# Kernel tuning notes

Hardware: AMD Instinct MI355X
Metric: run time of the kernel (lower is better)

Reference implementation:

```python
import jax, jax.numpy as jnp
import numpy as np

B, S, E, H = 2, 2048, 512, 8
D = E // H  # head_dim = 64


def setup_inputs() -> dict:
    key = jax.random.key(0)
    ks = jax.random.split(key, 10)
    sc = 1.0 / np.sqrt(E)
    x = jax.random.normal(ks[0], (B, S, E), dtype=jnp.float32)
    # parent index per node: tree_structure[b][parent[b,i]] contains i
    parent = jax.random.randint(ks[1], (B, S), 0, S, dtype=jnp.int32)
    Wp = jax.random.normal(ks[2], (E, E), dtype=jnp.float32) * sc
    bp = jnp.zeros((E,), dtype=jnp.float32)
    Wc = jax.random.normal(ks[3], (E, E), dtype=jnp.float32) * sc
    bc = jnp.zeros((E,), dtype=jnp.float32)
    Ws = jax.random.normal(ks[4], (E, E), dtype=jnp.float32) * sc
    bs = jnp.zeros((E,), dtype=jnp.float32)
    Wo = jax.random.normal(ks[5], (E, E), dtype=jnp.float32) * sc
    bo = jnp.zeros((E,), dtype=jnp.float32)
    return {"x": x, "parent": parent, "Wp": Wp, "bp": bp, "Wc": Wc,
            "bc": bc, "Ws": Ws, "bs": bs, "Wo": Wo, "bo": bo}


def _tree_mask(parent):
    # Vectorized equivalent of the per-batch scatter loop:
    # mask[b, p, c] = mask[b, c, p] = 1 for each (parent, child) edge.
    b_idx = jnp.arange(B)[:, None]
    rows = jnp.arange(S)[None, :]
    m = jnp.zeros((B, S, S), dtype=bool)
    m = m.at[b_idx, rows, parent].set(True)
    m = m.at[b_idx, parent, rows].set(True)
    return m  # (B, S, S), broadcast over heads


def reference(x, parent, Wp, bp, Wc, bc, Ws, bs, Wo, bo):
    # Tri-projection
    p = (x @ Wp + bp).reshape(B, S, H, D)
    c = (x @ Wc + bc).reshape(B, S, H, D)
    s = (x @ Ws + bs).reshape(B, S, H, D)
    scores = jnp.einsum('bnhd,bmhd->bnhm', p, c) / jnp.sqrt(jnp.float32(D))
    mask = _tree_mask(parent)  # (B, S, S)
    scores = jnp.where(mask[:, :, None, :], scores, -jnp.inf)
    attn = jax.nn.softmax(scores, axis=-1)  # dropout is identity (train=False)
    out = jnp.einsum('bnhm,bmhd->bnhd', attn, s).reshape(B, S, E)
    return out @ Wo + bo
```

## Files before the change

kernel.cpp:

```cpp
#include <hip/hip_runtime.h>
#include <hip/hip_bf16.h>

#define B_  2
#define S_  2048
#define E_  512
#define H_  8
#define D_  64
#define BS_ (B_ * S_)
#define N1_ 1536
#define K_  512

typedef __bf16 bf16x8 __attribute__((ext_vector_type(8)));
typedef float  f32x4  __attribute__((ext_vector_type(4)));

__device__ __forceinline__ ushort f2bf(float f) {
    unsigned u = __float_as_uint(f);
    unsigned r = (u + 0x7FFFu + ((u >> 16) & 1u)) >> 16;
    return (ushort)r;
}
__device__ __forceinline__ float bf2f(ushort b) {
    return __uint_as_float(((unsigned)b) << 16);
}

__device__ __forceinline__ float wave_sum(float v) {
    #pragma unroll
    for (int off = 32; off; off >>= 1) v += __shfl_xor(v, off);
    return v;
}

__device__ __forceinline__ void gld_lds16(const ushort* g, ushort* l) {
    __builtin_amdgcn_global_load_lds(
        (const __attribute__((address_space(1))) unsigned int*)g,
        (__attribute__((address_space(3))) unsigned int*)l, 16, 0, 0);
}


__global__ void convert_x_kernel(const float* __restrict__ x,
                                 ushort* __restrict__ xb, int n4) {
    int i = blockIdx.x * blockDim.x + threadIdx.x;
    if (i >= n4) return;
    float4 v = ((const float4*)x)[i];
    ushort4 o;
    o.x = f2bf(v.x); o.y = f2bf(v.y); o.z = f2bf(v.z); o.w = f2bf(v.w);
    ((ushort4*)xb)[i] = o;
}

__global__ __launch_bounds__(256) void transpose_all_kernel(
    const float* __restrict__ Wp, const float* __restrict__ Wc,
    const float* __restrict__ Ws, const float* __restrict__ Wo,
    ushort* __restrict__ Wcat_t, ushort* __restrict__ Wo_t) {
    __shared__ ushort T[64][65];
    int z = blockIdx.z;
    const float* src = (z == 0) ? Wp : (z == 1) ? Wc : (z == 2) ? Ws : Wo;
    ushort* dst = (z < 3) ? (Wcat_t + (size_t)z * 512 * 512) : Wo_t;
    int n0 = blockIdx.x * 64, k0 = blockIdx.y * 64;
    int tid = threadIdx.x;
    int g = tid >> 6, l = tid & 63;
    #pragma unroll
    for (int r = 0; r < 16; r++) {
        int kk = g * 16 + r;
        T[kk][l] = f2bf(src[(size_t)(k0 + kk) * 512 + n0 + l]);
    }
    __syncthreads();
    #pragma unroll
    for (int r = 0; r < 16; r++) {
        int nn = g * 16 + r;
        dst[(size_t)(n0 + nn) * 512 + k0 + l] = T[l][nn];
    }
}

template<int TN, bool BF16OUT>
__global__ __launch_bounds__(256) void gemm_mfma_kernel(
    const ushort* __restrict__ A,
    const ushort* __restrict__ Bt,
    const float*  __restrict__ b0,
    const float*  __restrict__ b1,
    const float*  __restrict__ b2,
    void* __restrict__ Cv,
    int N, int K) {
    constexpr int TM = 128, TK = 64;
    constexpr int NF = TN / 32;
    __shared__ ushort As[TM][TK];
    __shared__ ushort Bs[TN][TK];

    const int tid  = threadIdx.x;
    const int lane = tid & 63;
    const int wave = tid >> 6;
    const int wm = wave >> 1, wn = wave & 1;
    const int row0 = blockIdx.y * TM;
    const int col0 = blockIdx.x * TN;

    f32x4 acc[4][NF] = {};

    const int srow = lane >> 3;
    const int scol = (lane & 7) * 8;

    const int lrow = lane & 15;
    const int lk   = (lane >> 4) * 8;

    for (int kt = 0; kt < K; kt += TK) {
        const ushort* ga = A + (size_t)(row0 + wave * 32 + srow) * K + kt + scol;
        #pragma unroll
        for (int j = 0; j < 4; j++)
            gld_lds16(ga + (size_t)j * 8 * K, &As[wave * 32 + j * 8][0]);
        const ushort* gb = Bt + (size_t)(col0 + wave * (TN / 4) + srow) * K + kt + scol;
        #pragma unroll
        for (int j = 0; j < NF; j++)
            gld_lds16(gb + (size_t)j * 8 * K, &Bs[wave * (TN / 4) + j * 8][0]);
        __syncthreads();

        #pragma unroll
        for (int kk = 0; kk < TK; kk += 32) {
            bf16x8 af[4], bfr[NF];
            #pragma unroll
            for (int i = 0; i < 4; i++)
                af[i] = *(const bf16x8*)(&As[wm * 64 + i * 16 + lrow][kk + lk]);
            #pragma unroll
            for (int j = 0; j < NF; j++)
                bfr[j] = *(const bf16x8*)(&Bs[wn * (TN / 2) + j * 16 + lrow][kk + lk]);
            #pragma unroll
            for (int i = 0; i < 4; i++)
                #pragma unroll
                for (int j = 0; j < NF; j++)
                    acc[i][j] = __builtin_amdgcn_mfma_f32_16x16x32_bf16(
                        af[i], bfr[j], acc[i][j], 0, 0, 0);
        }
        __syncthreads();
    }

    const int ccol = lane & 15;
    const int crow = (lane >> 4) * 4;
    #pragma unroll
    for (int j = 0; j < NF; j++) {
        int gcol = col0 + wn * (TN / 2) + j * 16 + ccol;
        float bias = (gcol < 512) ? b0[gcol]
                   : (gcol < 1024) ? b1[gcol - 512] : b2[gcol - 1024];
        #pragma unroll
        for (int i = 0; i < 4; i++) {
            int grow = row0 + wm * 64 + i * 16 + crow;
            #pragma unroll
            for (int rg = 0; rg < 4; rg++) {
                float v = acc[i][j][rg] + bias;
                if (BF16OUT)
                    ((ushort*)Cv)[(size_t)(grow + rg) * N + gcol] = f2bf(v);
                else
                    ((float*)Cv)[(size_t)(grow + rg) * N + gcol] = v;
            }
        }
    }
}

__global__ __launch_bounds__(256) void attn_gather_kernel(
    const ushort* __restrict__ PCS, const int* __restrict__ parent,
    ushort* __restrict__ attn) {
    int gtid = blockIdx.x * blockDim.x + threadIdx.x;
    int w    = gtid >> 6;
    int lane = gtid & 63;
    int bbase = ((w >> 11) << 11);
    int i  = w & (S_ - 1);
    int rp = bbase + parent[w];

    float pn[H_];
    #pragma unroll
    for (int h = 0; h < H_; h++)
        pn[h] = bf2f(PCS[(size_t)w * N1_ + h * 64 + lane]);

    float Zh[H_], avh[H_];
    {
        const ushort* rm = PCS + (size_t)rp * N1_;
        #pragma unroll
        for (int h = 0; h < H_; h++) {
            float cm = bf2f(rm[512 + h * 64 + lane]);
            float sm = bf2f(rm[1024 + h * 64 + lane]);
            float sc = wave_sum(pn[h] * cm);
            float e = __expf(sc * 0.125f);
            Zh[h]  = e;
            avh[h] = e * sm;
        }
    }

    for (int t0 = 0; t0 < S_; t0 += 64) {
        int m = bbase + t0 + lane;
        unsigned long long mask = __ballot(parent[m] == i);
        while (mask) {
            int l = __ffsll(mask) - 1;
            mask &= mask - 1;
            int c = bbase + t0 + l;
            if (c == rp) continue;
            const ushort* rc = PCS + (size_t)c * N1_;
            #pragma unroll
            for (int h = 0; h < H_; h++) {
                float cc = bf2f(rc[512 + h * 64 + lane]);
                float sc = wave_sum(pn[h] * cc);
                float e = __expf(sc * 0.125f);
                Zh[h]  += e;
                avh[h] += e * bf2f(rc[1024 + h * 64 + lane]);
            }
        }
    }

    #pragma unroll
    for (int h = 0; h < H_; h++)
        attn[(size_t)w * E_ + h * 64 + lane] = f2bf(avh[h] / Zh[h]);
}

extern "C" void kernel_launch(void* const* d_in, const int* in_sizes, int n_in,
                              void* d_out, int out_size, void* d_ws, size_t ws_size,
                              hipStream_t stream) {
    const float* x      = (const float*)d_in[0];
    const int*   parent = (const int*)  d_in[1];
    const float* Wp     = (const float*)d_in[2];
    const float* bp     = (const float*)d_in[3];
    const float* Wc     = (const float*)d_in[4];
    const float* bc     = (const float*)d_in[5];
    const float* Ws     = (const float*)d_in[6];
    const float* bs     = (const float*)d_in[7];
    const float* Wo     = (const float*)d_in[8];
    const float* bo     = (const float*)d_in[9];
    float* out = (float*)d_out;

    char* ws = (char*)d_ws;
    ushort* x_bf    = (ushort*)(ws + 0);
    ushort* Wcat_t  = (ushort*)(ws + 4194304);
    ushort* Wo_t    = (ushort*)(ws + 5767168);
    ushort* PCS_bf  = (ushort*)(ws + 6291456);
    ushort* attn_bf = (ushort*)(ws + 18874368);

    convert_x_kernel<<<(BS_ * E_ / 4 + 255) / 256, 256, 0, stream>>>(
        x, x_bf, BS_ * E_ / 4);
    transpose_all_kernel<<<dim3(8, 8, 4), 256, 0, stream>>>(
        Wp, Wc, Ws, Wo, Wcat_t, Wo_t);

    gemm_mfma_kernel<128, true><<<dim3(N1_ / 128, BS_ / 128), 256, 0, stream>>>(
        x_bf, Wcat_t, bp, bc, bs, PCS_bf, N1_, K_);

    attn_gather_kernel<<<BS_ * 64 / 256, 256, 0, stream>>>(
        PCS_bf, parent, attn_bf);

    gemm_mfma_kernel<64, false><<<dim3(E_ / 64, BS_ / 128), 256, 0, stream>>>(
        attn_bf, Wo_t, bo, bo, bo, out, E_, K_);
}
```

Baseline: 125.3 us.

## Merge prep kernels, vectorize parent scan, shrink QKV GEMM tile width

Fuses the x-to-bf16 conversion and weight transpose kernels into one launch with a flat block index, removing one kernel launch. The child scan in the attention gather kernel now loads four parent indices per lane via int4, covering 256 nodes per iteration with four ballots instead of one ballot per 64. The fused QKV projection GEMM uses a 64-wide N tile, doubling its grid to improve CU occupancy at the cost of less B-tile reuse.

```diff
diff --git a/kernel.cpp b/kernel.cpp
--- a/kernel.cpp
+++ b/kernel.cpp
@@ -34,27 +34,28 @@
         (__attribute__((address_space(3))) unsigned int*)l, 16, 0, 0);
 }
 
-
-__global__ void convert_x_kernel(const float* __restrict__ x,
-                                 ushort* __restrict__ xb, int n4) {
-    int i = blockIdx.x * blockDim.x + threadIdx.x;
-    if (i >= n4) return;
-    float4 v = ((const float4*)x)[i];
-    ushort4 o;
-    o.x = f2bf(v.x); o.y = f2bf(v.y); o.z = f2bf(v.z); o.w = f2bf(v.w);
-    ((ushort4*)xb)[i] = o;
-}
-
-__global__ __launch_bounds__(256) void transpose_all_kernel(
+__global__ __launch_bounds__(256) void prep_kernel(
+    const float* __restrict__ x, ushort* __restrict__ xb,
     const float* __restrict__ Wp, const float* __restrict__ Wc,
     const float* __restrict__ Ws, const float* __restrict__ Wo,
     ushort* __restrict__ Wcat_t, ushort* __restrict__ Wo_t) {
+    int bid = blockIdx.x;
+    int tid = threadIdx.x;
+    if (bid < 2048) {
+        int i = bid * 256 + tid;
+        float4 v = ((const float4*)x)[i];
+        ushort4 o;
+        o.x = f2bf(v.x); o.y = f2bf(v.y); o.z = f2bf(v.z); o.w = f2bf(v.w);
+        ((ushort4*)xb)[i] = o;
+        return;
+    }
     __shared__ ushort T[64][65];
-    int z = blockIdx.z;
+    int bid2 = bid - 2048;
+    int z = bid2 >> 6;
+    int t = bid2 & 63;
     const float* src = (z == 0) ? Wp : (z == 1) ? Wc : (z == 2) ? Ws : Wo;
     ushort* dst = (z < 3) ? (Wcat_t + (size_t)z * 512 * 512) : Wo_t;
-    int n0 = blockIdx.x * 64, k0 = blockIdx.y * 64;
-    int tid = threadIdx.x;
+    int n0 = (t & 7) * 64, k0 = (t >> 3) * 64;
     int g = tid >> 6, l = tid & 63;
     #pragma unroll
     for (int r = 0; r < 16; r++) {
@@ -179,22 +180,26 @@
         }
     }
 
-    for (int t0 = 0; t0 < S_; t0 += 64) {
-        int m = bbase + t0 + lane;
-        unsigned long long mask = __ballot(parent[m] == i);
-        while (mask) {
-            int l = __ffsll(mask) - 1;
-            mask &= mask - 1;
-            int c = bbase + t0 + l;
-            if (c == rp) continue;
-            const ushort* rc = PCS + (size_t)c * N1_;
-            #pragma unroll
-            for (int h = 0; h < H_; h++) {
-                float cc = bf2f(rc[512 + h * 64 + lane]);
-                float sc = wave_sum(pn[h] * cc);
-                float e = __expf(sc * 0.125f);
-                Zh[h]  += e;
-                avh[h] += e * bf2f(rc[1024 + h * 64 + lane]);
+    for (int t0 = 0; t0 < S_; t0 += 256) {
+        int4 pv = *(const int4*)(parent + bbase + t0 + lane * 4);
+        int pc[4] = {pv.x, pv.y, pv.z, pv.w};
+        #pragma unroll
+        for (int jj = 0; jj < 4; jj++) {
+            unsigned long long mask = __ballot(pc[jj] == i);
+            while (mask) {
+                int l = __ffsll(mask) - 1;
+                mask &= mask - 1;
+                int c = bbase + t0 + l * 4 + jj;
+                if (c == rp) continue;
+                const ushort* rc = PCS + (size_t)c * N1_;
+                #pragma unroll
+                for (int h = 0; h < H_; h++) {
+                    float cc = bf2f(rc[512 + h * 64 + lane]);
+                    float sc = wave_sum(pn[h] * cc);
+                    float e = __expf(sc * 0.125f);
+                    Zh[h]  += e;
+                    avh[h] += e * bf2f(rc[1024 + h * 64 + lane]);
+                }
             }
         }
     }
@@ -226,12 +231,9 @@
     ushort* PCS_bf  = (ushort*)(ws + 6291456);
     ushort* attn_bf = (ushort*)(ws + 18874368);
 
-    convert_x_kernel<<<(BS_ * E_ / 4 + 255) / 256, 256, 0, stream>>>(
-        x, x_bf, BS_ * E_ / 4);
-    transpose_all_kernel<<<dim3(8, 8, 4), 256, 0, stream>>>(
-        Wp, Wc, Ws, Wo, Wcat_t, Wo_t);
-
-    gemm_mfma_kernel<128, true><<<dim3(N1_ / 128, BS_ / 128), 256, 0, stream>>>(
+    prep_kernel<<<2304, 256, 0, stream>>>(x, x_bf, Wp, Wc, Ws, Wo, Wcat_t, Wo_t);
+
+    gemm_mfma_kernel<64, true><<<dim3(N1_ / 64, BS_ / 128), 256, 0, stream>>>(
         x_bf, Wcat_t, bp, bc, bs, PCS_bf, N1_, K_);
 
     attn_gather_kernel<<<BS_ * 64 / 256, 256, 0, stream>>>(
```

Measured after the change: 120.1 us. 4.2% less time.
